# Kernel tuning notes

Measured on AMD Instinct MI355X. Metric: run time of the kernel, lower is better.

## Reference

```python
import jax, jax.numpy as jnp
import numpy as np

B, S, D, H = 2, 2048, 2048, 16
HD = D // H  # head_dim = 128
ROPE_BASE = 10000.0


def _rope_interleaved(x, cos, sin):
    # x: [B, S, H, HD]; cos/sin: [S, HD//2]
    xe = x[..., 0::2]
    xo = x[..., 1::2]
    c = cos[None, :, None, :]
    s = sin[None, :, None, :]
    oe = xe * c - xo * s
    oo = xe * s + xo * c
    # re-interleave pairs back to last dim
    return jnp.stack([oe, oo], axis=-1).reshape(x.shape)


def setup_inputs() -> dict:
    key = jax.random.key(0)
    k0, k1, k2, k3 = jax.random.split(key, 4)
    scale = D ** -0.5
    x = jax.random.normal(k0, (B, S, D), dtype=jnp.float32)
    wqk = jax.random.normal(k1, (2 * D, D), dtype=jnp.float32) * scale
    wv = jax.random.normal(k2, (D, D), dtype=jnp.float32) * scale
    wo = jax.random.normal(k3, (D, D), dtype=jnp.float32) * scale
    return {"x": x, "wqk": wqk, "wv": wv, "wo": wo}


def reference(x, wqk, wv, wo):
    b, s, d = x.shape
    # fused QK projection -> [B, S, 2, H, HD]
    xqk = (x @ wqk.T).reshape(b, s, 2, H, HD)
    xq = xqk[:, :, 0]
    xk = xqk[:, :, 1]
    xv = (x @ wv.T).reshape(b, s, H, HD)

    # interleaved rotary embedding (seqlen_offset=0, no-cache path)
    inv_freq = 1.0 / (ROPE_BASE ** (jnp.arange(0, HD, 2, dtype=jnp.float32) / HD))
    freqs = jnp.arange(s, dtype=jnp.float32)[:, None] * inv_freq[None, :]  # [S, HD//2]
    cos, sin = jnp.cos(freqs), jnp.sin(freqs)
    xq = _rope_interleaved(xq, cos, sin)
    xk = _rope_interleaved(xk, cos, sin)

    # causal scaled-dot-product attention
    scores = jnp.einsum("bqhd,bkhd->bhqk", xq, xk) * (HD ** -0.5)
    causal = jnp.tril(jnp.ones((s, s), dtype=bool))
    scores = jnp.where(causal[None, None], scores, jnp.finfo(scores.dtype).min)
    probs = jax.nn.softmax(scores, axis=-1)
    out = jnp.einsum("bhqk,bkhd->bqhd", probs, xv).reshape(b, s, d)
    return out @ wo.T
```

## Files before the change

### kernel.cpp

```cpp
#include <hip/hip_runtime.h>
#include <hip/hip_bf16.h>

#define NB 2
#define SEQ 2048
#define DMODEL 2048
#define NH 16
#define HD 128
#define QSCALE (0.08838834764831845f * 1.44269504088896f)
#define THRL2 11.5f

using bf16x8 = __attribute__((ext_vector_type(8))) __bf16;
using f32x4  = __attribute__((ext_vector_type(4))) float;

#define MFMA16 __builtin_amdgcn_mfma_f32_16x16x32_bf16

typedef __attribute__((address_space(1))) const void* gptr_t;
typedef __attribute__((address_space(3))) void* lptr_t;

__device__ inline void gload_lds16(const unsigned short* g, unsigned short* l) {
    __builtin_amdgcn_global_load_lds((gptr_t)g, (lptr_t)l, 16, 0, 0);
}

__device__ inline unsigned short f2b(float f) {
    unsigned u = __builtin_bit_cast(unsigned, f);
    u += 0x7FFF + ((u >> 16) & 1);
    return (unsigned short)(u >> 16);
}
__device__ inline float b2f(unsigned short h) {
    return __builtin_bit_cast(float, (unsigned)h << 16);
}
__device__ inline float fexp2(float x) {
    float r;
    asm("v_exp_f32 %0, %1" : "=v"(r) : "v"(x));
    return r;
}
__device__ inline unsigned cvtpk(float a, float b) {
    unsigned r;
    asm("v_cvt_pk_bf16_f32 %0, %1, %2" : "=v"(r) : "v"(a), "v"(b));
    return r;
}

__global__ void cast_f2b(const float* __restrict__ src, unsigned short* __restrict__ dst, int n) {
    int i = (blockIdx.x * 256 + threadIdx.x) * 4;
    if (i + 3 < n) {
        float4 v = *reinterpret_cast<const float4*>(src + i);
        ushort4 o;
        o.x = f2b(v.x); o.y = f2b(v.y); o.z = f2b(v.z); o.w = f2b(v.w);
        *reinterpret_cast<ushort4*>(dst + i) = o;
    }
}

__global__ void rope_tab(float2* __restrict__ tab) {
    int idx = blockIdx.x * 256 + threadIdx.x;
    int i = idx & 63;
    int s = idx >> 6;
    float inv = exp2f(-13.287712379549449f * (float)i * (1.0f / 64.0f));
    float ang = (float)s * inv;
    float sn, cs;
    sincosf(ang, &sn, &cs);
    tab[idx] = make_float2(cs, sn);
}

template<int MODE>
__global__ __launch_bounds__(512) void gemm8p(const unsigned short* __restrict__ A,
                                              const unsigned short* __restrict__ Bw,
                                              void* __restrict__ Cout,
                                              unsigned short* __restrict__ qb,
                                              unsigned short* __restrict__ kbp,
                                              unsigned short* __restrict__ vx,
                                              const float2* __restrict__ tab,
                                              int M, int N, int K) {
    __shared__ __align__(16) char lds[98304];
    int tid = threadIdx.x;
    int lane = tid & 63;
    int wid = tid >> 6;
    int wm = wid >> 2, wn = wid & 3;
    int row0 = blockIdx.y * 128;
    int col0 = blockIdx.x * 256;
    int lr = lane & 15, g = lane >> 4;

    const unsigned short* srcA[2];
    const unsigned short* srcB[4];
#pragma unroll
    for (int i = 0; i < 2; i++) {
        int chunk = i * 512 + tid;
        int ksub = chunk >> 9;
        int cw = chunk & 511;
        int row = cw >> 2, c = cw & 3;
        int cs = c ^ ((row >> 1) & 3);
        srcA[i] = A + (size_t)(row0 + row) * K + ksub * 32 + cs * 8;
    }
#pragma unroll
    for (int i = 0; i < 4; i++) {
        int chunk = i * 512 + tid;
        int ksub = chunk >> 10;
        int cw = chunk & 1023;
        int row = cw >> 2, c = cw & 3;
        int cs = c ^ ((row >> 1) & 3);
        srcB[i] = Bw + (size_t)(col0 + row) * K + ksub * 32 + cs * 8;
    }

    int offA[4][2], offB[4][2];
#pragma unroll
    for (int i = 0; i < 4; i++) {
        int row = wm * 64 + i * 16 + lr;
#pragma unroll
        for (int ks = 0; ks < 2; ks++)
            offA[i][ks] = ks * 8192 + row * 64 + ((g ^ ((row >> 1) & 3)) * 16);
    }
#pragma unroll
    for (int j = 0; j < 4; j++) {
        int row = wn * 64 + j * 16 + lr;
#pragma unroll
        for (int ks = 0; ks < 2; ks++)
            offB[j][ks] = ks * 16384 + row * 64 + ((g ^ ((row >> 1) & 3)) * 16);
    }

    f32x4 acc[4][4] = {};
    int NT = K >> 6;

#define STAGE8(t) {                                                                   \
        int kb_ = (t) * 64;                                                           \
        int bs_ = ((t) & 1) * 49152;                                                  \
        _Pragma("unroll")                                                             \
        for (int i_ = 0; i_ < 2; i_++)                                                \
            gload_lds16(srcA[i_] + kb_,                                               \
                (unsigned short*)(lds + bs_ + (i_ * 512 + (tid & ~63)) * 16));        \
        _Pragma("unroll")                                                             \
        for (int i_ = 0; i_ < 4; i_++)                                                \
            gload_lds16(srcB[i_] + kb_,                                               \
                (unsigned short*)(lds + bs_ + 16384 + (i_ * 512 + (tid & ~63)) * 16)); \
    }

    STAGE8(0);
    for (int t = 0; t < NT; ++t) {
        if (t + 1 < NT) {
            STAGE8(t + 1);
            asm volatile("s_waitcnt vmcnt(6)" ::: "memory");
        } else {
            asm volatile("s_waitcnt vmcnt(0)" ::: "memory");
        }
        __builtin_amdgcn_s_barrier();
        __builtin_amdgcn_sched_barrier(0);

        const char* ab = lds + (t & 1) * 49152;
        const char* bb = ab + 16384;

        bf16x8 b[4][2], a[2][2];
#pragma unroll
        for (int j = 0; j < 4; j++)
#pragma unroll
            for (int ks = 0; ks < 2; ks++)
                b[j][ks] = *reinterpret_cast<const bf16x8*>(bb + offB[j][ks]);
#pragma unroll
        for (int i = 0; i < 2; i++)
#pragma unroll
            for (int ks = 0; ks < 2; ks++)
                a[i][ks] = *reinterpret_cast<const bf16x8*>(ab + offA[i][ks]);
        asm volatile("s_waitcnt lgkmcnt(0)" ::: "memory");
        __builtin_amdgcn_sched_barrier(0);
        __builtin_amdgcn_s_setprio(1);
#pragma unroll
        for (int ks = 0; ks < 2; ks++)
#pragma unroll
            for (int i = 0; i < 2; i++)
#pragma unroll
                for (int j = 0; j < 4; j++)
                    acc[i][j] = MFMA16(a[i][ks], b[j][ks], acc[i][j], 0, 0, 0);
        __builtin_amdgcn_s_setprio(0);

        bf16x8 a2[2][2];
#pragma unroll
        for (int i = 0; i < 2; i++)
#pragma unroll
            for (int ks = 0; ks < 2; ks++)
                a2[i][ks] = *reinterpret_cast<const bf16x8*>(ab + offA[2 + i][ks]);
        asm volatile("s_waitcnt lgkmcnt(0)" ::: "memory");
        __builtin_amdgcn_sched_barrier(0);
        __builtin_amdgcn_s_barrier();
        __builtin_amdgcn_sched_barrier(0);
        __builtin_amdgcn_s_setprio(1);
#pragma unroll
        for (int ks = 0; ks < 2; ks++)
#pragma unroll
            for (int i = 0; i < 2; i++)
#pragma unroll
                for (int j = 0; j < 4; j++)
                    acc[2 + i][j] = MFMA16(a2[i][ks], b[j][ks], acc[2 + i][j], 0, 0, 0);
        __builtin_amdgcn_s_setprio(0);
    }
#undef STAGE8

    int orow = g * 4;
    if (MODE == 0) {
#pragma unroll
        for (int i = 0; i < 4; i++) {
#pragma unroll
            for (int j = 0; j < 4; j++) {
                int r0 = row0 + wm * 64 + i * 16 + orow;
                int c  = col0 + wn * 64 + j * 16 + lr;
#pragma unroll
                for (int r = 0; r < 4; r++)
                    ((float*)Cout)[(size_t)(r0 + r) * N + c] = acc[i][j][r];
            }
        }
    } else {
        int bx = blockIdx.x;
        if (bx < 16) {
            const bool isQ = (bx < 8);
            unsigned short* dst = isQ ? qb : kbp;
#pragma unroll
            for (int i = 0; i < 4; i++) {
#pragma unroll
                for (int j = 0; j < 4; j++) {
                    int c = col0 + wn * 64 + j * 16 + lr;
                    int cc = c & 2047;
                    int h = cc >> 7, d = cc & 127, i2 = d >> 1;
                    int odd = lr & 1;
#pragma unroll
                    for (int r = 0; r < 4; r++) {
                        int trow = row0 + wm * 64 + i * 16 + orow + r;
                        int s = trow & (SEQ - 1), bb2 = trow >> 11;
                        float v = acc[i][j][r];
                        float pv = __shfl_xor(v, 1);
                        float2 cssn = tab[s * 64 + i2];
                        float out = odd ? (pv * cssn.y + v * cssn.x)
                                        : (v * cssn.x - pv * cssn.y);
                        if (isQ) out *= QSCALE;
                        dst[((size_t)((bb2 * NH + h) * SEQ + s)) * HD + d] = f2b(out);
                    }
                }
            }
        } else {
#pragma unroll
            for (int i = 0; i < 4; i++) {
#pragma unroll
                for (int j = 0; j < 4; j++) {
                    int cc = col0 + wn * 64 + j * 16 + lr - 4096;
#pragma unroll
                    for (int r = 0; r < 4; r++) {
                        int trow = row0 + wm * 64 + i * 16 + orow + r;
                        vx[(size_t)trow * 2048 + cc] = f2b(acc[i][j][r]);
                    }
                }
            }
        }
    }
}

__global__ __launch_bounds__(256) void v_tr(const unsigned short* __restrict__ vx,
                                            unsigned short* __restrict__ vt) {
    __shared__ unsigned short tl[64][68];
    int bid = blockIdx.x;
    int st = bid & 31;
    int dt = (bid >> 5) & 1;
    int bh = bid >> 6;
    int b = bh >> 4, h = bh & 15;
    int tid = threadIdx.x;
    int rr = tid >> 2;
    int rc = (tid & 3) * 16;

    const unsigned short* src = vx + (size_t)(b * SEQ + st * 64 + rr) * 2048 + h * HD + dt * 64 + rc;
    uint4 v0 = *reinterpret_cast<const uint4*>(src);
    uint4 v1 = *reinterpret_cast<const uint4*>(src + 8);
    *reinterpret_cast<uint4*>(&tl[rr][rc]) = v0;
    *reinterpret_cast<uint4*>(&tl[rr][rc + 8]) = v1;
    __syncthreads();

    unsigned short tmp[16];
#pragma unroll
    for (int k = 0; k < 16; k++) tmp[k] = tl[rc + k][rr];
    unsigned short* dst = vt + (size_t)(bh * HD + dt * 64 + rr) * SEQ + st * 64 + rc;
    *reinterpret_cast<uint4*>(dst)     = *reinterpret_cast<const uint4*>(&tmp[0]);
    *reinterpret_cast<uint4*>(dst + 8) = *reinterpret_cast<const uint4*>(&tmp[8]);
}

__global__ __launch_bounds__(64, 1) void attn6(const unsigned short* __restrict__ Q,
                                               const unsigned short* __restrict__ Kb,
                                               const unsigned short* __restrict__ Vt,
                                               unsigned short* __restrict__ O) {
    __shared__ __align__(16) char lds[36864];

    int lane = threadIdx.x;
    int bid = blockIdx.x;
    int p  = bid >> 5;
    int bh = bid & 31;
    int lr = lane & 15;
    int g  = lane >> 4;
    int g4 = g * 4;
    int lk = g * 8;

    const unsigned short* Qp = Q  + (size_t)bh * SEQ * HD;
    const unsigned short* Kp = Kb + (size_t)bh * SEQ * HD;
    const unsigned short* Vp = Vt + (size_t)bh * HD * SEQ;
    char* pl = lds + 32768;
    int b = bh >> 4;
    int h = bh & 15;

    int srcoff[16];
#pragma unroll
    for (int i2 = 0; i2 < 16; ++i2) {
        int r = i2 * 4 + g;
        srcoff[i2] = r * HD + ((lr ^ (r & 7)) * 8);
    }

#define STAGEK(bufbase, kvbase)                                                     \
    {                                                                               \
        const unsigned short* kbase = Kp + (size_t)(kvbase) * HD;                   \
        _Pragma("unroll")                                                           \
        for (int i2 = 0; i2 < 16; ++i2)                                             \
            gload_lds16(kbase + srcoff[i2],                                         \
                        (unsigned short*)(lds + (bufbase) + i2 * 1024));            \
    }

    for (int ph = 0; ph < 2; ++ph) {
        int j  = ph ? (63 - p) : p;
        int q0 = j * 32;
        int ktiles = (j >> 1) + 1;

        bf16x8 qf[2][4];
#pragma unroll
        for (int f = 0; f < 2; f++)
#pragma unroll
            for (int kb = 0; kb < 4; kb++)
                qf[f][kb] = *reinterpret_cast<const bf16x8*>(Qp + (size_t)(q0 + f * 16 + lr) * HD + kb * 32 + lk);

        f32x4 oacc[2][8] = {};
        float m[2] = { -1e30f, -1e30f }, l[2] = { 0.0f, 0.0f };
        int qrow[2] = { q0 + lr, q0 + 16 + lr };

        STAGEK(0, 0);

        int cur = 0;
        for (int t = 0; t < ktiles; ++t) {
            int kv0 = t * 64;
            if (t + 1 < ktiles) {
                STAGEK((cur ^ 1) * 16384, kv0 + 64);
                asm volatile("s_waitcnt vmcnt(16)" ::: "memory");
            } else {
                asm volatile("s_waitcnt vmcnt(0)" ::: "memory");
            }
            __builtin_amdgcn_sched_barrier(0);

            char* kb_c = lds + cur * 16384;
            f32x4 s[2][4] = {};
#pragma unroll
            for (int kb = 0; kb < 4; kb++) {
#pragma unroll
                for (int jj = 0; jj < 4; jj++) {
                    int row = jj * 16 + lr;
                    int cin = ((kb * 4 + g) ^ (row & 7));
                    bf16x8 kf = *reinterpret_cast<const bf16x8*>(kb_c + row * 256 + cin * 16);
                    s[0][jj] = MFMA16(kf, qf[0][kb], s[0][jj], 0, 0, 0);
                    s[1][jj] = MFMA16(kf, qf[1][kb], s[1][jj], 0, 0, 0);
                }
            }

            bf16x8 vf[8][2];
#pragma unroll
            for (int db = 0; db < 8; db++)
#pragma unroll
                for (int ks = 0; ks < 2; ks++)
                    vf[db][ks] = *reinterpret_cast<const bf16x8*>(Vp + (size_t)(db * 16 + lr) * SEQ + kv0 + ks * 32 + lk);

#pragma unroll
            for (int f = 0; f < 2; f++) {
                int q = qrow[f];
                bool full = (kv0 + 63 <= q0 + f * 16);
                float mx = -1e30f;
                if (full) {
#pragma unroll
                    for (int jj = 0; jj < 4; jj++)
#pragma unroll
                        for (int r = 0; r < 4; r++)
                            mx = fmaxf(mx, s[f][jj][r]);
                } else {
#pragma unroll
                    for (int jj = 0; jj < 4; jj++)
#pragma unroll
                        for (int r = 0; r < 4; r++) {
                            int kv = kv0 + jj * 16 + g4 + r;
                            float v = (kv <= q) ? s[f][jj][r] : -1e30f;
                            s[f][jj][r] = v;
                            mx = fmaxf(mx, v);
                        }
                }
                mx = fmaxf(mx, __shfl_xor(mx, 16));
                mx = fmaxf(mx, __shfl_xor(mx, 32));

                if (!__all(mx <= m[f] + THRL2)) {
                    float mn = fmaxf(m[f], mx);
                    float sc = fexp2(m[f] - mn);
                    m[f] = mn;
                    l[f] *= sc;
#pragma unroll
                    for (int db = 0; db < 8; db++)
#pragma unroll
                        for (int r = 0; r < 4; r++)
                            oacc[f][db][r] *= sc;
                }

                int row = f * 16 + lr;
                int rb = row * 128;
                int sw = (row & 7) << 4;
                float rs = 0.0f;
#pragma unroll
                for (int jj = 0; jj < 4; jj++)
#pragma unroll
                    for (int hh = 0; hh < 2; hh++) {
                        float p0 = fexp2(s[f][jj][2 * hh]     - m[f]);
                        float p1 = fexp2(s[f][jj][2 * hh + 1] - m[f]);
                        rs += p0 + p1;
                        unsigned pk = cvtpk(p0, p1);
                        int colb = jj * 32 + g * 8 + 4 * hh;
                        *reinterpret_cast<unsigned*>(pl + rb + (colb ^ sw)) = pk;
                    }
                rs += __shfl_xor(rs, 16);
                rs += __shfl_xor(rs, 32);
                l[f] += rs;
            }

            asm volatile("s_waitcnt lgkmcnt(0)" ::: "memory");
            __builtin_amdgcn_sched_barrier(0);

            bf16x8 pb[2][2];
#pragma unroll
            for (int f = 0; f < 2; f++)
#pragma unroll
                for (int ks = 0; ks < 2; ks++) {
                    int row = f * 16 + lr;
                    int off = row * 128 + ((ks * 64 + g * 16) ^ ((row & 7) << 4));
                    pb[f][ks] = *reinterpret_cast<const bf16x8*>(pl + off);
                }
#pragma unroll
            for (int db = 0; db < 8; db++)
#pragma unroll
                for (int ks = 0; ks < 2; ks++) {
                    oacc[0][db] = MFMA16(vf[db][ks], pb[0][ks], oacc[0][db], 0, 0, 0);
                    oacc[1][db] = MFMA16(vf[db][ks], pb[1][ks], oacc[1][db], 0, 0, 0);
                }

            cur ^= 1;
        }

#pragma unroll
        for (int f = 0; f < 2; f++) {
            float inv = 1.0f / l[f];
            int q = q0 + f * 16 + lr;
            unsigned short* op = O + ((size_t)(b * SEQ + q)) * DMODEL + h * HD;
#pragma unroll
            for (int db = 0; db < 8; db++) {
                ushort4 o4;
                o4.x = f2b(oacc[f][db][0] * inv);
                o4.y = f2b(oacc[f][db][1] * inv);
                o4.z = f2b(oacc[f][db][2] * inv);
                o4.w = f2b(oacc[f][db][3] * inv);
                *reinterpret_cast<ushort4*>(op + db * 16 + g4) = o4;
            }
        }
    }
#undef STAGEK
}

extern "C" void kernel_launch(void* const* d_in, const int* in_sizes, int n_in,
                              void* d_out, int out_size, void* d_ws, size_t ws_size,
                              hipStream_t stream) {
    const float* x   = (const float*)d_in[0];
    const float* wqk = (const float*)d_in[1];
    const float* wv  = (const float*)d_in[2];
    const float* wo  = (const float*)d_in[3];

    unsigned short* xb  = (unsigned short*)d_ws;
    unsigned short* wb  = xb  + (size_t)8388608;
    unsigned short* qb  = wb  + (size_t)16777216;
    unsigned short* kb  = qb  + (size_t)8388608;
    unsigned short* vx  = kb  + (size_t)8388608;
    unsigned short* vt  = vx  + (size_t)8388608;
    unsigned short* ao  = vt  + (size_t)8388608;
    float2* tab = (float2*)(ao + (size_t)8388608);

    cast_f2b<<<8192, 256, 0, stream>>>(x,   xb, 8388608);
    cast_f2b<<<8192, 256, 0, stream>>>(wqk, wb, 8388608);
    cast_f2b<<<4096, 256, 0, stream>>>(wv,  wb + 8388608, 4194304);
    cast_f2b<<<4096, 256, 0, stream>>>(wo,  wb + 12582912, 4194304);
    rope_tab<<<512, 256, 0, stream>>>(tab);

    gemm8p<2><<<dim3(24, 32), 512, 0, stream>>>(xb, wb, nullptr, qb, kb, vx, tab, 4096, 6144, 2048);

    v_tr<<<2048, 256, 0, stream>>>(vx, vt);

    attn6<<<1024, 64, 0, stream>>>(qb, kb, vt, ao);

    gemm8p<0><<<dim3(8, 32), 512, 0, stream>>>(ao, wb + 12582912, d_out, nullptr, nullptr, nullptr, nullptr, 4096, 2048, 2048);
}
```

Measured before the change: 283.2 us.

## Shrink attention KV tile to 32, one query tile per block, fuse cast kernels

The attention kernel changes from processing two paired query tiles per block with 64-row KV tiles to one 32-row query tile per block with 32-row KV tiles. That halves the LDS footprint, allows two blocks per CU, doubles the grid, and launches the heaviest tiles first. The four cast launches and the rope table launch are merged into a single kernel to cut launch overhead. Smaller KV tiles mean more loop iterations, more softmax and sync overhead per unit of work, and less MFMA work per iteration.

After: 279.5 us. Within noise of the previous version (-1.3%).

```diff
diff --git a/kernel.cpp b/kernel.cpp
--- a/kernel.cpp
+++ b/kernel.cpp
@@ -40,25 +40,32 @@
     return r;
 }
 
-__global__ void cast_f2b(const float* __restrict__ src, unsigned short* __restrict__ dst, int n) {
-    int i = (blockIdx.x * 256 + threadIdx.x) * 4;
-    if (i + 3 < n) {
+__global__ void cast_all(const float* __restrict__ x, const float* __restrict__ wqk,
+                         const float* __restrict__ wv, const float* __restrict__ wo,
+                         unsigned short* __restrict__ xb, unsigned short* __restrict__ wb,
+                         float2* __restrict__ tab) {
+    int idx = blockIdx.x * 256 + threadIdx.x;
+    if (idx < 6291456) {
+        const float* src; unsigned short* dst; int off;
+        if (idx < 2097152)      { src = x;   dst = xb;             off = 0; }
+        else if (idx < 4194304) { src = wqk; dst = wb;             off = 2097152; }
+        else if (idx < 5242880) { src = wv;  dst = wb + 8388608;   off = 4194304; }
+        else                    { src = wo;  dst = wb + 12582912;  off = 5242880; }
+        int i = (idx - off) * 4;
         float4 v = *reinterpret_cast<const float4*>(src + i);
         ushort4 o;
         o.x = f2b(v.x); o.y = f2b(v.y); o.z = f2b(v.z); o.w = f2b(v.w);
         *reinterpret_cast<ushort4*>(dst + i) = o;
-    }
-}
-
-__global__ void rope_tab(float2* __restrict__ tab) {
-    int idx = blockIdx.x * 256 + threadIdx.x;
-    int i = idx & 63;
-    int s = idx >> 6;
-    float inv = exp2f(-13.287712379549449f * (float)i * (1.0f / 64.0f));
-    float ang = (float)s * inv;
-    float sn, cs;
-    sincosf(ang, &sn, &cs);
-    tab[idx] = make_float2(cs, sn);
+    } else {
+        int k = idx - 6291456;
+        int i = k & 63;
+        int s = k >> 6;
+        float inv = exp2f(-13.287712379549449f * (float)i * (1.0f / 64.0f));
+        float ang = (float)s * inv;
+        float sn, cs;
+        sincosf(ang, &sn, &cs);
+        tab[k] = make_float2(cs, sn);
+    }
 }
 
 template<int MODE>
@@ -275,16 +282,18 @@
     *reinterpret_cast<uint4*>(dst + 8) = *reinterpret_cast<const uint4*>(&tmp[8]);
 }
 
-__global__ __launch_bounds__(64, 1) void attn6(const unsigned short* __restrict__ Q,
+__global__ __launch_bounds__(64, 2) void attn8(const unsigned short* __restrict__ Q,
                                                const unsigned short* __restrict__ Kb,
                                                const unsigned short* __restrict__ Vt,
                                                unsigned short* __restrict__ O) {
-    __shared__ __align__(16) char lds[36864];
+    __shared__ __align__(16) char lds[18432];
 
     int lane = threadIdx.x;
     int bid = blockIdx.x;
-    int p  = bid >> 5;
+    int qt = 63 - (bid >> 5);
     int bh = bid & 31;
+    int q0 = qt * 32;
+    int ktiles = qt + 1;
     int lr = lane & 15;
     int g  = lane >> 4;
     int g4 = g * 4;
@@ -293,173 +302,161 @@
     const unsigned short* Qp = Q  + (size_t)bh * SEQ * HD;
     const unsigned short* Kp = Kb + (size_t)bh * SEQ * HD;
     const unsigned short* Vp = Vt + (size_t)bh * HD * SEQ;
-    char* pl = lds + 32768;
+    char* pl = lds + 16384;
     int b = bh >> 4;
     int h = bh & 15;
 
-    int srcoff[16];
-#pragma unroll
-    for (int i2 = 0; i2 < 16; ++i2) {
+    int srcoff[8];
+#pragma unroll
+    for (int i2 = 0; i2 < 8; ++i2) {
         int r = i2 * 4 + g;
         srcoff[i2] = r * HD + ((lr ^ (r & 7)) * 8);
     }
 
-#define STAGEK(bufbase, kvbase)                                                     \
+#define STAGEK32(bufbase, kvbase)                                                   \
     {                                                                               \
         const unsigned short* kbase = Kp + (size_t)(kvbase) * HD;                   \
         _Pragma("unroll")                                                           \
-        for (int i2 = 0; i2 < 16; ++i2)                                             \
+        for (int i2 = 0; i2 < 8; ++i2)                                              \
             gload_lds16(kbase + srcoff[i2],                                         \
                         (unsigned short*)(lds + (bufbase) + i2 * 1024));            \
     }
 
-    for (int ph = 0; ph < 2; ++ph) {
-        int j  = ph ? (63 - p) : p;
-        int q0 = j * 32;
-        int ktiles = (j >> 1) + 1;
-
-        bf16x8 qf[2][4];
-#pragma unroll
-        for (int f = 0; f < 2; f++)
-#pragma unroll
-            for (int kb = 0; kb < 4; kb++)
-                qf[f][kb] = *reinterpret_cast<const bf16x8*>(Qp + (size_t)(q0 + f * 16 + lr) * HD + kb * 32 + lk);
-
-        f32x4 oacc[2][8] = {};
-        float m[2] = { -1e30f, -1e30f }, l[2] = { 0.0f, 0.0f };
-        int qrow[2] = { q0 + lr, q0 + 16 + lr };
-
-        STAGEK(0, 0);
-
-        int cur = 0;
-        for (int t = 0; t < ktiles; ++t) {
-            int kv0 = t * 64;
-            if (t + 1 < ktiles) {
-                STAGEK((cur ^ 1) * 16384, kv0 + 64);
-                asm volatile("s_waitcnt vmcnt(16)" ::: "memory");
+    bf16x8 qf[2][4];
+#pragma unroll
+    for (int f = 0; f < 2; f++)
+#pragma unroll
+        for (int kb = 0; kb < 4; kb++)
+            qf[f][kb] = *reinterpret_cast<const bf16x8*>(Qp + (size_t)(q0 + f * 16 + lr) * HD + kb * 32 + lk);
+
+    f32x4 oacc[2][8] = {};
+    float m[2] = { -1e30f, -1e30f }, l[2] = { 0.0f, 0.0f };
+    int qrow[2] = { q0 + lr, q0 + 16 + lr };
+
+    STAGEK32(0, 0);
+
+    int cur = 0;
+    for (int t = 0; t < ktiles; ++t) {
+        int kv0 = t * 32;
+        if (t + 1 < ktiles) {
+            STAGEK32((cur ^ 1) * 8192, kv0 + 32);
+            asm volatile("s_waitcnt vmcnt(8)" ::: "memory");
+        } else {
+            asm volatile("s_waitcnt vmcnt(0)" ::: "memory");
+        }
+        __builtin_amdgcn_sched_barrier(0);
+
+        char* kb_c = lds + cur * 8192;
+        f32x4 s[2][2] = {};
+#pragma unroll
+        for (int kb = 0; kb < 4; kb++) {
+#pragma unroll
+            for (int jj = 0; jj < 2; jj++) {
+                int row = jj * 16 + lr;
+                int cin = ((kb * 4 + g) ^ (row & 7));
+                bf16x8 kf = *reinterpret_cast<const bf16x8*>(kb_c + row * 256 + cin * 16);
+                s[0][jj] = MFMA16(kf, qf[0][kb], s[0][jj], 0, 0, 0);
+                s[1][jj] = MFMA16(kf, qf[1][kb], s[1][jj], 0, 0, 0);
+            }
+        }
+
+        bf16x8 vf[8];
+#pragma unroll
+        for (int db = 0; db < 8; db++)
+            vf[db] = *reinterpret_cast<const bf16x8*>(Vp + (size_t)(db * 16 + lr) * SEQ + kv0 + lk);
+
+#pragma unroll
+        for (int f = 0; f < 2; f++) {
+            int q = qrow[f];
+            bool full = (kv0 + 31 <= q0 + f * 16);
+            float mx = -1e30f;
+            if (full) {
+#pragma unroll
+                for (int jj = 0; jj < 2; jj++)
+#pragma unroll
+                    for (int r = 0; r < 4; r++)
+                        mx = fmaxf(mx, s[f][jj][r]);
             } else {
-                asm volatile("s_waitcnt vmcnt(0)" ::: "memory");
-            }
-            __builtin_amdgcn_sched_barrier(0);
-
-            char* kb_c = lds + cur * 16384;
-            f32x4 s[2][4] = {};
-#pragma unroll
-            for (int kb = 0; kb < 4; kb++) {
-#pragma unroll
-                for (int jj = 0; jj < 4; jj++) {
-                    int row = jj * 16 + lr;
-                    int cin = ((kb * 4 + g) ^ (row & 7));
-                    bf16x8 kf = *reinterpret_cast<const bf16x8*>(kb_c + row * 256 + cin * 16);
-                    s[0][jj] = MFMA16(kf, qf[0][kb], s[0][jj], 0, 0, 0);
-                    s[1][jj] = MFMA16(kf, qf[1][kb], s[1][jj], 0, 0, 0);
+#pragma unroll
+                for (int jj = 0; jj < 2; jj++)
+#pragma unroll
+                    for (int r = 0; r < 4; r++) {
+                        int kv = kv0 + jj * 16 + g4 + r;
+                        float v = (kv <= q) ? s[f][jj][r] : -1e30f;
+                        s[f][jj][r] = v;
+                        mx = fmaxf(mx, v);
+                    }
+            }
+            mx = fmaxf(mx, __shfl_xor(mx, 16));
+            mx = fmaxf(mx, __shfl_xor(mx, 32));
+
+            if (!__all(mx <= m[f] + THRL2)) {
+                float mn = fmaxf(m[f], mx);
+                float sc = fexp2(m[f] - mn);
+                m[f] = mn;
+                l[f] *= sc;
+#pragma unroll
+                for (int db = 0; db < 8; db++)
+#pragma unroll
+                    for (int r = 0; r < 4; r++)
+                        oacc[f][db][r] *= sc;
+            }
+
+            int row = f * 16 + lr;
+            int rb = row * 64;
+            int sw = (row & 3) << 4;
+            float rs = 0.0f;
+#pragma unroll
+            for (int jj = 0; jj < 2; jj++)
+#pragma unroll
+                for (int hh = 0; hh < 2; hh++) {
+                    float p0 = fexp2(s[f][jj][2 * hh]     - m[f]);
+                    float p1 = fexp2(s[f][jj][2 * hh + 1] - m[f]);
+                    rs += p0 + p1;
+                    unsigned pk = cvtpk(p0, p1);
+                    int colb = jj * 32 + g * 8 + 4 * hh;
+                    *reinterpret_cast<unsigned*>(pl + rb + (colb ^ sw)) = pk;
                 }
-            }
-
-            bf16x8 vf[8][2];
-#pragma unroll
-            for (int db = 0; db < 8; db++)
-#pragma unroll
-                for (int ks = 0; ks < 2; ks++)
-                    vf[db][ks] = *reinterpret_cast<const bf16x8*>(Vp + (size_t)(db * 16 + lr) * SEQ + kv0 + ks * 32 + lk);
-
-#pragma unroll
-            for (int f = 0; f < 2; f++) {
-                int q = qrow[f];
-                bool full = (kv0 + 63 <= q0 + f * 16);
-                float mx = -1e30f;
-                if (full) {
-#pragma unroll
-                    for (int jj = 0; jj < 4; jj++)
-#pragma unroll
-                        for (int r = 0; r < 4; r++)
-                            mx = fmaxf(mx, s[f][jj][r]);
-                } else {
-#pragma unroll
-                    for (int jj = 0; jj < 4; jj++)
-#pragma unroll
-                        for (int r = 0; r < 4; r++) {
-                            int kv = kv0 + jj * 16 + g4 + r;
-                            float v = (kv <= q) ? s[f][jj][r] : -1e30f;
-                            s[f][jj][r] = v;
-                            mx = fmaxf(mx, v);
-                        }
-                }
-                mx = fmaxf(mx, __shfl_xor(mx, 16));
-                mx = fmaxf(mx, __shfl_xor(mx, 32));
-
-                if (!__all(mx <= m[f] + THRL2)) {
-                    float mn = fmaxf(m[f], mx);
-                    float sc = fexp2(m[f] - mn);
-                    m[f] = mn;
-                    l[f] *= sc;
-#pragma unroll
-                    for (int db = 0; db < 8; db++)
-#pragma unroll
-                        for (int r = 0; r < 4; r++)
-                            oacc[f][db][r] *= sc;
-                }
-
-                int row = f * 16 + lr;
-                int rb = row * 128;
-                int sw = (row & 7) << 4;
-                float rs = 0.0f;
-#pragma unroll
-                for (int jj = 0; jj < 4; jj++)
-#pragma unroll
-                    for (int hh = 0; hh < 2; hh++) {
-                        float p0 = fexp2(s[f][jj][2 * hh]     - m[f]);
-                        float p1 = fexp2(s[f][jj][2 * hh + 1] - m[f]);
-                        rs += p0 + p1;
-                        unsigned pk = cvtpk(p0, p1);
-                        int colb = jj * 32 + g * 8 + 4 * hh;
-                        *reinterpret_cast<unsigned*>(pl + rb + (colb ^ sw)) = pk;
-                    }
-                rs += __shfl_xor(rs, 16);
-                rs += __shfl_xor(rs, 32);
-                l[f] += rs;
-            }
-
-            asm volatile("s_waitcnt lgkmcnt(0)" ::: "memory");
-            __builtin_amdgcn_sched_barrier(0);
-
-            bf16x8 pb[2][2];
-#pragma unroll
-            for (int f = 0; f < 2; f++)
-#pragma unroll
-                for (int ks = 0; ks < 2; ks++) {
-                    int row = f * 16 + lr;
-                    int off = row * 128 + ((ks * 64 + g * 16) ^ ((row & 7) << 4));
-                    pb[f][ks] = *reinterpret_cast<const bf16x8*>(pl + off);
-                }
-#pragma unroll
-            for (int db = 0; db < 8; db++)
-#pragma unroll
-                for (int ks = 0; ks < 2; ks++) {
-                    oacc[0][db] = MFMA16(vf[db][ks], pb[0][ks], oacc[0][db], 0, 0, 0);
-                    oacc[1][db] = MFMA16(vf[db][ks], pb[1][ks], oacc[1][db], 0, 0, 0);
-                }
-
-            cur ^= 1;
-        }
-
+            rs += __shfl_xor(rs, 16);
+            rs += __shfl_xor(rs, 32);
+            l[f] += rs;
+        }
+
+        asm volatile("s_waitcnt lgkmcnt(0)" ::: "memory");
+        __builtin_amdgcn_sched_barrier(0);
+
+        bf16x8 pb[2];
 #pragma unroll
         for (int f = 0; f < 2; f++) {
-            float inv = 1.0f / l[f];
-            int q = q0 + f * 16 + lr;
-            unsigned short* op = O + ((size_t)(b * SEQ + q)) * DMODEL + h * HD;
-#pragma unroll
-            for (int db = 0; db < 8; db++) {
-                ushort4 o4;
-                o4.x = f2b(oacc[f][db][0] * inv);
-                o4.y = f2b(oacc[f][db][1] * inv);
-                o4.z = f2b(oacc[f][db][2] * inv);
-                o4.w = f2b(oacc[f][db][3] * inv);
-                *reinterpret_cast<ushort4*>(op + db * 16 + g4) = o4;
-            }
-        }
-    }
-#undef STAGEK
+            int row = f * 16 + lr;
+            int off = row * 64 + ((g * 16) ^ ((row & 3) << 4));
+            pb[f] = *reinterpret_cast<const bf16x8*>(pl + off);
+        }
+#pragma unroll
+        for (int db = 0; db < 8; db++) {
+            oacc[0][db] = MFMA16(vf[db], pb[0], oacc[0][db], 0, 0, 0);
+            oacc[1][db] = MFMA16(vf[db], pb[1], oacc[1][db], 0, 0, 0);
+        }
+
+        cur ^= 1;
+    }
+
+#pragma unroll
+    for (int f = 0; f < 2; f++) {
+        float inv = 1.0f / l[f];
+        int q = q0 + f * 16 + lr;
+        unsigned short* op = O + ((size_t)(b * SEQ + q)) * DMODEL + h * HD;
+#pragma unroll
+        for (int db = 0; db < 8; db++) {
+            ushort4 o4;
+            o4.x = f2b(oacc[f][db][0] * inv);
+            o4.y = f2b(oacc[f][db][1] * inv);
+            o4.z = f2b(oacc[f][db][2] * inv);
+            o4.w = f2b(oacc[f][db][3] * inv);
+            *reinterpret_cast<ushort4*>(op + db * 16 + g4) = o4;
+        }
+    }
+#undef STAGEK32
 }
 
 extern "C" void kernel_launch(void* const* d_in, const int* in_sizes, int n_in,
@@ -479,17 +476,13 @@
     unsigned short* ao  = vt  + (size_t)8388608;
     float2* tab = (float2*)(ao + (size_t)8388608);
 
-    cast_f2b<<<8192, 256, 0, stream>>>(x,   xb, 8388608);
-    cast_f2b<<<8192, 256, 0, stream>>>(wqk, wb, 8388608);
-    cast_f2b<<<4096, 256, 0, stream>>>(wv,  wb + 8388608, 4194304);
-    cast_f2b<<<4096, 256, 0, stream>>>(wo,  wb + 12582912, 4194304);
-    rope_tab<<<512, 256, 0, stream>>>(tab);
+    cast_all<<<25088, 256, 0, stream>>>(x, wqk, wv, wo, xb, wb, tab);
 
     gemm8p<2><<<dim3(24, 32), 512, 0, stream>>>(xb, wb, nullptr, qb, kb, vx, tab, 4096, 6144, 2048);
 
     v_tr<<<2048, 256, 0, stream>>>(vx, vt);
 
-    attn6<<<1024, 64, 0, stream>>>(qb, kb, vt, ao);
+    attn8<<<2048, 64, 0, stream>>>(qb, kb, vt, ao);
 
     gemm8p<0><<<dim3(8, 32), 512, 0, stream>>>(ao, wb + 12582912, d_out, nullptr, nullptr, nullptr, nullptr, 4096, 2048, 2048);
 }
```
